# Optimization experiments

Hardware: AMD Instinct MI355X
Metric: run time of the kernel (lower is better)

## Reference

```python
import jax, jax.numpy as jnp
import numpy as np

B, N, D, H = 8, 1024, 1024, 16
DK = D // H


def setup_inputs() -> dict:
    key = jax.random.key(0)
    ks = jax.random.split(key, 5)
    s_in = 1.0 / np.sqrt(D)
    return {
        "x": jax.random.normal(ks[0], (B, N, D), dtype=jnp.float32),
        "w_qkv": jax.random.uniform(ks[1], (D, 3 * D), jnp.float32, -s_in, s_in),
        "b_qkv": jax.random.uniform(ks[2], (3 * D,), jnp.float32, -s_in, s_in),
        "w_proj": jax.random.uniform(ks[3], (D, D), jnp.float32, -s_in, s_in),
        "b_proj": jax.random.uniform(ks[4], (D,), jnp.float32, -s_in, s_in),
    }


def reference(x, w_qkv, b_qkv, w_proj, b_proj):
    # x: (B, N, D)
    qkv = x @ w_qkv + b_qkv                      # (B, N, 3D)
    q, k, v = jnp.split(qkv, 3, axis=-1)
    # reshape to (B, H, N, DK)
    def heads(t):
        return t.reshape(B, N, H, DK).transpose(0, 2, 1, 3)
    q, k, v = heads(q), heads(k), heads(v)
    scale = 1.0 / np.sqrt(DK).astype(np.float32)
    scores = jnp.einsum("bhnd,bhmd->bhnm", q, k) * scale  # (B, H, N, N)
    attn = jax.nn.softmax(scores, axis=-1)
    out = jnp.einsum("bhnm,bhmd->bhnd", attn, v)          # (B, H, N, DK)
    out = out.transpose(0, 2, 1, 3).reshape(B, N, D)
    return out @ w_proj + b_proj
```

## Files before the change

### kernel.cpp

```cpp
#include <hip/hip_runtime.h>
#include <hip/hip_bf16.h>


#define BB 8
#define NN 1024
#define DD 1024
#define HH 16
#define DK 64
#define TOK (BB * NN)
#define QKVN (3 * DD)

typedef __attribute__((ext_vector_type(8))) short bf16x8;
typedef __attribute__((ext_vector_type(4))) float f32x4;
typedef __attribute__((ext_vector_type(4))) short short4v;
typedef __attribute__((ext_vector_type(4))) float float4v;

static __device__ __forceinline__ short f2bf(float f) {
  union { float f; unsigned u; } v; v.f = f;
  unsigned r = (v.u + 0x7FFFu + ((v.u >> 16) & 1u)) >> 16;
  return (short)r;
}
static __device__ __forceinline__ short f2bf_rn(float f) {
  __hip_bfloat16 h(f);
  short s;
  __builtin_memcpy(&s, &h, 2);
  return s;
}
static __device__ __forceinline__ float fexp2(float x) {
#if __has_builtin(__builtin_amdgcn_exp2f)
  return __builtin_amdgcn_exp2f(x);
#else
  return __expf(x * 0.69314718056f);
#endif
}

static __device__ __forceinline__ void gload_lds16(const short* g, short* lds, int lane) {
#if __has_builtin(__builtin_amdgcn_global_load_lds)
  __builtin_amdgcn_global_load_lds((const __attribute__((address_space(1))) void*)g,
                                   (__attribute__((address_space(3))) void*)lds, 16, 0, 0);
#else
  ((bf16x8*)lds)[lane] = *(const bf16x8*)g;
#endif
}

__global__ __launch_bounds__(256) void cast_f32_bf16(const float* __restrict__ in,
                                                     short* __restrict__ out, long n) {
  long i = ((long)blockIdx.x * blockDim.x + threadIdx.x) * 4;
  if (i >= n) return;
  float4v v = *(const float4v*)(in + i);
  short4v o;
  o[0] = f2bf(v[0]); o[1] = f2bf(v[1]); o[2] = f2bf(v[2]); o[3] = f2bf(v[3]);
  *(short4v*)(out + i) = o;
}

__global__ __launch_bounds__(256) void transpose_cast(const float* __restrict__ in,
                                                      short* __restrict__ out,
                                                      int rows, int cols) {
  __shared__ float tile[32][33];
  int bx = blockIdx.x * 32;
  int by = blockIdx.y * 32;
  int tx = threadIdx.x, ty = threadIdx.y;
#pragma unroll
  for (int q = 0; q < 4; q++)
    tile[ty + 8 * q][tx] = in[(long)(by + ty + 8 * q) * cols + bx + tx];
  __syncthreads();
#pragma unroll
  for (int q = 0; q < 4; q++)
    out[(long)(bx + ty + 8 * q) * rows + by + tx] = f2bf(tile[tx][ty + 8 * q]);
}

template <int MODE>
__global__ __launch_bounds__(256) void gemm_bt(const short* __restrict__ A,
                                               const short* __restrict__ Bt,
                                               const float* __restrict__ bias,
                                               void* __restrict__ Cout,
                                               short* __restrict__ vT,
                                               int M, int N, int K, int ldc) {
  __shared__ __align__(16) short As[2][128 * 32];
  __shared__ __align__(16) short Bs[2][128 * 32];
  const int tid = threadIdx.x;
  const int w = tid >> 6, lane = tid & 63;
  const int r = lane & 15, g = lane >> 4;
  const int wm = w >> 1, wn = w & 1;

  const int nwg = gridDim.x * gridDim.y;
  const int flat = blockIdx.y * gridDim.x + blockIdx.x;
  const int swz = (flat & 7) * (nwg >> 3) + (flat >> 3);
  const int bx = swz % gridDim.x, by = swz / gridDim.x;

  const long tileM = (long)by * 128;
  const long tileN = (long)bx * 128;

  f32x4 acc[4][4] = {};

  const int rowInChunk = lane >> 2;
  const int colOff = ((lane & 3) ^ ((lane >> 3) & 3)) * 8;
  const int rdChunk = (g ^ ((r >> 1) & 3)) * 8;

  const int nt = K >> 5;
#pragma unroll
  for (int issue = 0; issue < 2; ++issue) {
    int c = w * 2 + issue;
    gload_lds16(A + (tileM + c * 16 + rowInChunk) * (long)K + colOff, &As[0][c * 512], lane);
    gload_lds16(Bt + (tileN + c * 16 + rowInChunk) * (long)K + colOff, &Bs[0][c * 512], lane);
  }
  __syncthreads();

  for (int t = 0; t < nt; ++t) {
    const int cur = t & 1;
    if (t + 1 < nt) {
      const int k0 = (t + 1) << 5;
#pragma unroll
      for (int issue = 0; issue < 2; ++issue) {
        int c = w * 2 + issue;
        gload_lds16(A + (tileM + c * 16 + rowInChunk) * (long)K + k0 + colOff,
                    &As[cur ^ 1][c * 512], lane);
        gload_lds16(Bt + (tileN + c * 16 + rowInChunk) * (long)K + k0 + colOff,
                    &Bs[cur ^ 1][c * 512], lane);
      }
    }

    bf16x8 a[4], b[4];
#pragma unroll
    for (int i = 0; i < 4; i++)
      a[i] = *(const bf16x8*)&As[cur][(wm * 64 + i * 16 + r) * 32 + rdChunk];
#pragma unroll
    for (int i = 0; i < 4; i++)
      b[i] = *(const bf16x8*)&Bs[cur][(wn * 64 + i * 16 + r) * 32 + rdChunk];
#pragma unroll
    for (int i = 0; i < 4; i++)
#pragma unroll
      for (int ii = 0; ii < 4; ii++)
        acc[i][ii] = __builtin_amdgcn_mfma_f32_16x16x32_bf16(a[i], b[ii], acc[i][ii], 0, 0, 0);

    __syncthreads();
  }

#pragma unroll
  for (int i = 0; i < 4; i++) {
    long rowb = tileM + wm * 64 + i * 16 + g * 4;
#pragma unroll
    for (int ii = 0; ii < 4; ii++) {
      long cn = tileN + wn * 64 + ii * 16 + r;
      float bv = bias[cn];
      float v0 = acc[i][ii][0] + bv;
      float v1 = acc[i][ii][1] + bv;
      float v2 = acc[i][ii][2] + bv;
      float v3 = acc[i][ii][3] + bv;
      if constexpr (MODE == 0) {
        float* C = (float*)Cout;
        C[(rowb + 0) * ldc + cn] = v0;
        C[(rowb + 1) * ldc + cn] = v1;
        C[(rowb + 2) * ldc + cn] = v2;
        C[(rowb + 3) * ldc + cn] = v3;
      } else {
        if (cn < 2048) {
          short* C = (short*)Cout;
          C[(rowb + 0) * ldc + cn] = f2bf(v0);
          C[(rowb + 1) * ldc + cn] = f2bf(v1);
          C[(rowb + 2) * ldc + cn] = f2bf(v2);
          C[(rowb + 3) * ldc + cn] = f2bf(v3);
        } else {
          int hc = (int)(cn - 2048);
          int b = (int)(rowb >> 10);
          int n0 = (int)(rowb & 1023);
          int pos = (n0 & ~31) + 8 * ((n0 >> 2) & 3) + 4 * ((n0 >> 4) & 1);
          long va = ((long)(b * 16 + (hc >> 6)) * 64 + (hc & 63)) * 1024 + pos;
          short4v sv;
          sv[0] = f2bf(v0); sv[1] = f2bf(v1); sv[2] = f2bf(v2); sv[3] = f2bf(v3);
          *(short4v*)&vT[va] = sv;
        }
      }
    }
  }
}

__global__ __launch_bounds__(256) void attn_kernel(const short* __restrict__ qk,
                                                   const short* __restrict__ vT,
                                                   short* __restrict__ attn_out) {
  __shared__ __align__(16) short Ks[64 * 64];
  __shared__ __align__(16) short Vs[64 * 64];

  const int nwg = gridDim.x * gridDim.y;
  const int flat = blockIdx.y * gridDim.x + blockIdx.x;
  const int swz = (flat & 7) * (nwg >> 3) + (flat >> 3);
  const int bh = swz >> 3;
  const int qt = swz & 7;

  const int bb = bh >> 4, h = bh & 15;
  const int tid = threadIdx.x;
  const int wid = tid >> 6, lane = tid & 63;
  const int r = lane & 15, g = lane >> 4;
  const int qbase = qt * 128 + wid * 32;
  const int RS = 2048;
  const long base = (long)bb * NN * RS;
  const short* Qp = qk + base + h * 64;
  const short* Kp = qk + base + DD + h * 64;
  const short* vTh = vT + (long)bh * 64 * 1024;

  const int srow0 = 8 * wid + (lane >> 3);
  const int sj = (lane & 7) ^ (lane >> 3);

  bf16x8 qf[2][2];
#pragma unroll
  for (int qg = 0; qg < 2; qg++) {
    const short* qrow = Qp + (long)(qbase + 16 * qg + r) * RS;
    qf[qg][0] = *(const bf16x8*)(qrow + 8 * g);
    qf[qg][1] = *(const bf16x8*)(qrow + 32 + 8 * g);
  }

  const float C = 0.18033688f;
  float m2[2] = {-3e38f, -3e38f}, lsum[2] = {0.0f, 0.0f};
  f32x4 o[2][4] = {};

  for (int kv0 = 0; kv0 < NN; kv0 += 64) {
    __syncthreads();
#pragma unroll
    for (int i = 0; i < 2; i++) {
      int srow = 32 * i + srow0;
      gload_lds16(Kp + (long)(kv0 + srow) * RS + sj * 8, &Ks[i * 2048 + wid * 512], lane);
      gload_lds16(vTh + (long)srow * 1024 + kv0 + sj * 8, &Vs[i * 2048 + wid * 512], lane);
    }
    __syncthreads();

    bf16x8 kf[2][2][2];
#pragma unroll
    for (int c = 0; c < 2; c++)
#pragma unroll
      for (int u = 0; u < 2; u++) {
        int krow = 32 * c + 16 * u + r;
#pragma unroll
        for (int s = 0; s < 2; s++)
          kf[c][u][s] = *(const bf16x8*)&Ks[krow * 64 + (((4 * s + g) ^ (r & 7)) * 8)];
      }

    bf16x8 pf[2][2];
#pragma unroll
    for (int qg = 0; qg < 2; qg++) {
      f32x4 s[2][2];
      __builtin_amdgcn_s_setprio(1);
#pragma unroll
      for (int c = 0; c < 2; c++)
#pragma unroll
        for (int u = 0; u < 2; u++) {
          f32x4 t = {};
          t = __builtin_amdgcn_mfma_f32_16x16x32_bf16(kf[c][u][0], qf[qg][0], t, 0, 0, 0);
          s[c][u] = __builtin_amdgcn_mfma_f32_16x16x32_bf16(kf[c][u][1], qf[qg][1], t, 0, 0, 0);
        }
      __builtin_amdgcn_s_setprio(0);

      float s16[16];
#pragma unroll
      for (int c = 0; c < 2; c++)
#pragma unroll
        for (int j = 0; j < 4; j++) {
          s16[8 * c + j] = s[c][0][j];
          s16[8 * c + 4 + j] = s[c][1][j];
        }

      float t8[8];
#pragma unroll
      for (int j = 0; j < 8; j++) t8[j] = fmaxf(s16[j], s16[j + 8]);
#pragma unroll
      for (int j = 0; j < 4; j++) t8[j] = fmaxf(t8[j], t8[j + 4]);
      float tmax = fmaxf(fmaxf(t8[0], t8[1]), fmaxf(t8[2], t8[3]));
      tmax = fmaxf(tmax, __shfl_xor(tmax, 16));
      tmax = fmaxf(tmax, __shfl_xor(tmax, 32));
      float tm2 = tmax * C;

      if (!__all(tm2 <= m2[qg] + 11.5416f)) {
        float mnew = fmaxf(m2[qg], tm2);
        float corr = fexp2(m2[qg] - mnew);
#pragma unroll
        for (int t = 0; t < 4; t++)
#pragma unroll
          for (int j = 0; j < 4; j++) o[qg][t][j] *= corr;
        lsum[qg] *= corr;
        m2[qg] = mnew;
      }

      float pv[16];
#pragma unroll
      for (int j = 0; j < 16; j++) pv[j] = fexp2(fmaf(s16[j], C, -m2[qg]));
      float s8[8];
#pragma unroll
      for (int j = 0; j < 8; j++) s8[j] = pv[j] + pv[j + 8];
#pragma unroll
      for (int j = 0; j < 4; j++) s8[j] = s8[j] + s8[j + 4];
      float ps = (s8[0] + s8[1]) + (s8[2] + s8[3]);
      ps += __shfl_xor(ps, 16);
      ps += __shfl_xor(ps, 32);
      lsum[qg] += ps;
#pragma unroll
      for (int c = 0; c < 2; c++)
#pragma unroll
        for (int j = 0; j < 8; j++) pf[qg][c][j] = f2bf_rn(pv[8 * c + j]);
    }

#pragma unroll
    for (int t = 0; t < 4; t++) {
      int vrow = 16 * t + r;
#pragma unroll
      for (int c = 0; c < 2; c++) {
        bf16x8 vt = *(const bf16x8*)&Vs[vrow * 64 + (((4 * c + g) ^ (r & 7)) * 8)];
        __builtin_amdgcn_s_setprio(1);
        o[0][t] = __builtin_amdgcn_mfma_f32_16x16x32_bf16(vt, pf[0][c], o[0][t], 0, 0, 0);
        o[1][t] = __builtin_amdgcn_mfma_f32_16x16x32_bf16(vt, pf[1][c], o[1][t], 0, 0, 0);
        __builtin_amdgcn_s_setprio(0);
      }
    }
  }

#pragma unroll
  for (int qg = 0; qg < 2; qg++) {
    float inv = 1.0f / lsum[qg];
    long orow = (long)(bb * NN + qbase + 16 * qg + r) * DD + h * 64;
#pragma unroll
    for (int t = 0; t < 4; t++) {
      short4v svv;
#pragma unroll
      for (int j = 0; j < 4; j++) svv[j] = f2bf(o[qg][t][j] * inv);
      *(short4v*)&attn_out[orow + 16 * t + 4 * g] = svv;
    }
  }
}

extern "C" void kernel_launch(void* const* d_in, const int* in_sizes, int n_in,
                              void* d_out, int out_size, void* d_ws, size_t ws_size,
                              hipStream_t stream) {
  const float* x = (const float*)d_in[0];
  const float* w_qkv = (const float*)d_in[1];
  const float* b_qkv = (const float*)d_in[2];
  const float* w_proj = (const float*)d_in[3];
  const float* b_proj = (const float*)d_in[4];
  float* out = (float*)d_out;

  short* ws = (short*)d_ws;
  short* xb = ws;
  short* wqkvT = xb + (long)TOK * DD;
  short* wprojT = wqkvT + (long)QKVN * DD;
  short* qkb = wprojT + (long)DD * DD;
  short* vT = qkb + (long)TOK * 2048;
  short* attn = vT + (long)TOK * DD;

  cast_f32_bf16<<<(TOK * DD) / (256 * 4), 256, 0, stream>>>(x, xb, (long)TOK * DD);
  transpose_cast<<<dim3(QKVN / 32, DD / 32), dim3(32, 8), 0, stream>>>(w_qkv, wqkvT, DD, QKVN);
  transpose_cast<<<dim3(DD / 32, DD / 32), dim3(32, 8), 0, stream>>>(w_proj, wprojT, DD, DD);

  gemm_bt<1><<<dim3(QKVN / 128, TOK / 128), 256, 0, stream>>>(xb, wqkvT, b_qkv, qkb, vT,
                                                              TOK, QKVN, DD, 2048);

  attn_kernel<<<dim3(8, BB * HH), 256, 0, stream>>>(qkb, vT, attn);

  gemm_bt<0><<<dim3(DD / 128, TOK / 128), 256, 0, stream>>>(attn, wprojT, b_proj, out, nullptr,
                                                            TOK, DD, DD, DD);
}
```

Baseline: 184.0 us.

## Add 256x256-tile 512-thread pipelined GEMM for the QKV projection

Replaces the 128x128 QKV GEMM with a new 256x256-tile kernel using 8 waves, 64-wide K steps, swizzled LDS staging via direct global-to-LDS loads, and a double-buffered schedule with explicit vmcnt waits, barriers and setprio around MFMA groups. Larger tiles raise arithmetic intensity and cut global traffic, and the interleaved loads are meant to hide latency. The cost is 128KB of LDS per block, heavy register use and many barriers. The old MODE 1 V-transpose path is removed from gemm_bt, which is now used only for the output projection.

```diff
diff --git a/kernel.cpp b/kernel.cpp
--- a/kernel.cpp
+++ b/kernel.cpp
@@ -41,6 +41,12 @@
 #else
   ((bf16x8*)lds)[lane] = *(const bf16x8*)g;
 #endif
+}
+
+static __device__ __forceinline__ void block_barrier() {
+  asm volatile("" ::: "memory");
+  __builtin_amdgcn_s_barrier();
+  asm volatile("" ::: "memory");
 }
 
 __global__ __launch_bounds__(256) void cast_f32_bf16(const float* __restrict__ in,
@@ -67,6 +73,156 @@
 #pragma unroll
   for (int q = 0; q < 4; q++)
     out[(long)(bx + ty + 8 * q) * rows + by + tx] = f2bf(tile[tx][ty + 8 * q]);
+}
+
+__global__ __launch_bounds__(512, 2) void gemm256(const short* __restrict__ A,
+                                                  const short* __restrict__ Bt,
+                                                  const float* __restrict__ bias,
+                                                  short* __restrict__ Cqk,
+                                                  short* __restrict__ vT,
+                                                  int M, int N, int K, int ldc) {
+  __shared__ __align__(16) short lds[2][2][2][128 * 64];
+  const int tid = threadIdx.x;
+  const int wid = tid >> 6, lane = tid & 63;
+  const int r = lane & 15, g = lane >> 4;
+  const int wm = wid >> 2, wn = wid & 3;
+
+  const int nwg = gridDim.x * gridDim.y;
+  const int flat = blockIdx.y * gridDim.x + blockIdx.x;
+  const int swz = (flat & 7) * (nwg >> 3) + (flat >> 3);
+  const int bx = swz % gridDim.x, by = swz / gridDim.x;
+  const long tileM = (long)by * 256, tileN = (long)bx * 256;
+
+  f32x4 acc[8][4] = {};
+
+  const int sc = ((lane & 7) ^ ((lane >> 3) & 7)) * 8;
+  const int srl = lane >> 3;
+
+  const int akc0 = ((0 + g) ^ (r & 7)) * 8;
+  const int akc1 = ((4 + g) ^ (r & 7)) * 8;
+  const int bn0 = (wn & 1) * 64;
+  const int bh = wn >> 1;
+
+#define STAGEA(buf, h, Tt)                                                          \
+  {                                                                                 \
+    _Pragma("unroll") for (int j = 0; j < 2; j++)                                   \
+      gload_lds16(A + (tileM + (h) * 128 + wid * 16 + j * 8 + srl) * (long)K +      \
+                      (Tt) * 64 + sc,                                               \
+                  &lds[buf][0][h][(wid * 2 + j) * 512], lane);                      \
+  }
+#define STAGEB(buf, h, Tt)                                                          \
+  {                                                                                 \
+    _Pragma("unroll") for (int j = 0; j < 2; j++)                                   \
+      gload_lds16(Bt + (tileN + (h) * 128 + wid * 16 + j * 8 + srl) * (long)K +     \
+                      (Tt) * 64 + sc,                                               \
+                  &lds[buf][1][h][(wid * 2 + j) * 512], lane);                      \
+  }
+#define READ_A(q, p)                                                                \
+  af[0][0] = *(const bf16x8*)&lds[q][0][wm][((p) * 32 + r) * 64 + akc0];            \
+  af[0][1] = *(const bf16x8*)&lds[q][0][wm][((p) * 32 + r) * 64 + akc1];            \
+  af[1][0] = *(const bf16x8*)&lds[q][0][wm][((p) * 32 + 16 + r) * 64 + akc0];       \
+  af[1][1] = *(const bf16x8*)&lds[q][0][wm][((p) * 32 + 16 + r) * 64 + akc1];
+#define READ_B(q)                                                                   \
+  {                                                                                 \
+    const short* Bh = &lds[q][1][bh][0];                                            \
+    _Pragma("unroll") for (int fn = 0; fn < 4; fn++) {                              \
+      bf[fn][0] = *(const bf16x8*)&Bh[(bn0 + fn * 16 + r) * 64 + akc0];             \
+      bf[fn][1] = *(const bf16x8*)&Bh[(bn0 + fn * 16 + r) * 64 + akc1];             \
+    }                                                                               \
+  }
+#define MFMA_P(p)                                                                   \
+  __builtin_amdgcn_s_setprio(1);                                                    \
+  _Pragma("unroll") for (int fmi = 0; fmi < 2; fmi++)                               \
+      _Pragma("unroll") for (int fn = 0; fn < 4; fn++) {                            \
+    acc[2 * (p) + fmi][fn] = __builtin_amdgcn_mfma_f32_16x16x32_bf16(               \
+        af[fmi][0], bf[fn][0], acc[2 * (p) + fmi][fn], 0, 0, 0);                    \
+    acc[2 * (p) + fmi][fn] = __builtin_amdgcn_mfma_f32_16x16x32_bf16(               \
+        af[fmi][1], bf[fn][1], acc[2 * (p) + fmi][fn], 0, 0, 0);                    \
+  }                                                                                 \
+  __builtin_amdgcn_s_setprio(0);
+
+  const int NT = K >> 6;
+  const int NIT = NT >> 1;
+
+  STAGEA(0, 0, 0); STAGEA(0, 1, 0); STAGEB(0, 0, 0); STAGEB(0, 1, 0);
+  STAGEB(1, 0, 1); STAGEB(1, 1, 1);
+  asm volatile("s_waitcnt vmcnt(4)" ::: "memory");
+  block_barrier();
+
+  for (int i = 0; i < NIT; ++i) {
+    const int t1 = 2 * i + 1, t2 = 2 * i + 2, t3 = 2 * i + 3;
+    const bool full = (i < NIT - 1);
+    bf16x8 af[2][2], bf[4][2];
+
+    READ_A(0, 0); READ_B(0);
+    STAGEA(1, 0, t1);
+    block_barrier(); MFMA_P(0); block_barrier();
+
+    READ_A(0, 1);
+    STAGEA(1, 1, t1);
+    block_barrier(); MFMA_P(1); block_barrier();
+
+    READ_A(0, 2);
+    if (full) STAGEB(0, 0, t2);
+    block_barrier(); MFMA_P(2); block_barrier();
+
+    READ_A(0, 3);
+    if (full) STAGEB(0, 1, t2);
+    if (full) asm volatile("s_waitcnt vmcnt(4)" ::: "memory");
+    else      asm volatile("s_waitcnt vmcnt(0)" ::: "memory");
+    block_barrier(); MFMA_P(3); block_barrier();
+
+    READ_A(1, 0); READ_B(1);
+    if (full) STAGEA(0, 0, t2);
+    block_barrier(); MFMA_P(0); block_barrier();
+
+    READ_A(1, 1);
+    if (full) STAGEA(0, 1, t2);
+    block_barrier(); MFMA_P(1); block_barrier();
+
+    READ_A(1, 2);
+    if (full) STAGEB(1, 0, t3);
+    block_barrier(); MFMA_P(2); block_barrier();
+
+    READ_A(1, 3);
+    if (full) STAGEB(1, 1, t3);
+    if (full) asm volatile("s_waitcnt vmcnt(4)" ::: "memory");
+    block_barrier(); MFMA_P(3); block_barrier();
+  }
+#undef STAGEA
+#undef STAGEB
+#undef READ_A
+#undef READ_B
+#undef MFMA_P
+
+#pragma unroll
+  for (int fm = 0; fm < 8; fm++) {
+    long rowb = tileM + wm * 128 + fm * 16 + g * 4;
+#pragma unroll
+    for (int fn = 0; fn < 4; fn++) {
+      long cn = tileN + wn * 64 + fn * 16 + r;
+      float bv = bias[cn];
+      float v0 = acc[fm][fn][0] + bv;
+      float v1 = acc[fm][fn][1] + bv;
+      float v2 = acc[fm][fn][2] + bv;
+      float v3 = acc[fm][fn][3] + bv;
+      if (cn < 2048) {
+        Cqk[(rowb + 0) * ldc + cn] = f2bf(v0);
+        Cqk[(rowb + 1) * ldc + cn] = f2bf(v1);
+        Cqk[(rowb + 2) * ldc + cn] = f2bf(v2);
+        Cqk[(rowb + 3) * ldc + cn] = f2bf(v3);
+      } else {
+        int hc = (int)(cn - 2048);
+        int b = (int)(rowb >> 10);
+        int n0 = (int)(rowb & 1023);
+        int pos = (n0 & ~31) + 8 * ((n0 >> 2) & 3) + 4 * ((n0 >> 4) & 1);
+        long va = ((long)(b * 16 + (hc >> 6)) * 64 + (hc & 63)) * 1024 + pos;
+        short4v sv;
+        sv[0] = f2bf(v0); sv[1] = f2bf(v1); sv[2] = f2bf(v2); sv[3] = f2bf(v3);
+        *(short4v*)&vT[va] = sv;
+      }
+    }
+  }
 }
 
 template <int MODE>
@@ -154,22 +310,11 @@
         C[(rowb + 2) * ldc + cn] = v2;
         C[(rowb + 3) * ldc + cn] = v3;
       } else {
-        if (cn < 2048) {
-          short* C = (short*)Cout;
-          C[(rowb + 0) * ldc + cn] = f2bf(v0);
-          C[(rowb + 1) * ldc + cn] = f2bf(v1);
-          C[(rowb + 2) * ldc + cn] = f2bf(v2);
-          C[(rowb + 3) * ldc + cn] = f2bf(v3);
-        } else {
-          int hc = (int)(cn - 2048);
-          int b = (int)(rowb >> 10);
-          int n0 = (int)(rowb & 1023);
-          int pos = (n0 & ~31) + 8 * ((n0 >> 2) & 3) + 4 * ((n0 >> 4) & 1);
-          long va = ((long)(b * 16 + (hc >> 6)) * 64 + (hc & 63)) * 1024 + pos;
-          short4v sv;
-          sv[0] = f2bf(v0); sv[1] = f2bf(v1); sv[2] = f2bf(v2); sv[3] = f2bf(v3);
-          *(short4v*)&vT[va] = sv;
-        }
+        short* C = (short*)Cout;
+        C[(rowb + 0) * ldc + cn] = f2bf(v0);
+        C[(rowb + 1) * ldc + cn] = f2bf(v1);
+        C[(rowb + 2) * ldc + cn] = f2bf(v2);
+        C[(rowb + 3) * ldc + cn] = f2bf(v3);
       }
     }
   }
@@ -347,8 +492,8 @@
   transpose_cast<<<dim3(QKVN / 32, DD / 32), dim3(32, 8), 0, stream>>>(w_qkv, wqkvT, DD, QKVN);
   transpose_cast<<<dim3(DD / 32, DD / 32), dim3(32, 8), 0, stream>>>(w_proj, wprojT, DD, DD);
 
-  gemm_bt<1><<<dim3(QKVN / 128, TOK / 128), 256, 0, stream>>>(xb, wqkvT, b_qkv, qkb, vT,
-                                                              TOK, QKVN, DD, 2048);
+  gemm256<<<dim3(QKVN / 256, TOK / 256), 512, 0, stream>>>(xb, wqkvT, b_qkv, qkb, vT,
+                                                           TOK, QKVN, DD, 2048);
 
   attn_kernel<<<dim3(8, BB * HH), 256, 0, stream>>>(qkb, vT, attn);
 
```

Measured after the change: 180.1 us. -2.1%, faster.
